# Kernel tuning notes

Measured on AMD Instinct MI355X. Metric: run time of the kernel, lower is better.

Reference implementation:

```python
import jax, jax.numpy as jnp
import numpy as np

STRIDE, PAD, DIL = 1, 1, 1
EPS = 1e-12
RHO_LIM = 1.0 - 1e-6
PI = jnp.pi


def clamp_pg(x, lo=0.0):
    # clamp value but pass gradient through (clamp_preserve_grad)
    return x + jax.lax.stop_gradient(jnp.maximum(x, lo) - x)


def setup_inputs() -> dict:
    key = jax.random.key(0)
    B, N, T, K = 8, 128, 1024, 3
    k = jax.random.uniform(key, (B, B, N, T, 2), dtype=jnp.float32)
    leak = jnp.array(1.0, dtype=jnp.float32)
    alpha = jnp.full((1, 1, K), 1.0 / K, dtype=jnp.float32)
    beta = jnp.array(0.0, dtype=jnp.float32)
    return {"k": k, "leak": leak, "alpha": alpha, "beta": beta}


def reference(k, leak, alpha, beta):
    k_gp, k_ntk = k[..., 0], k[..., 1]          # (B,B,N,T) each
    B, _, N, T = k_gp.shape

    # v[b,t] = k_gp[b,b,0,t]  (diagonal over batch dims, first lag)
    ar = jnp.arange(B)
    v = k_gp[ar, ar, 0, :]                      # (B,T)
    v_pad = jnp.pad(v, ((0, 0), (0, N - 1)))    # (B, T+N-1)

    v_xx = v[:, None, None, :]                  # (B,1,1,T)
    idx = jnp.arange(N)[:, None] + jnp.arange(T)[None, :]  # (N,T)
    v_yy = v_pad[:, idx][None]                  # (1,B,N,T): v_pad[b, n+t]

    # calculate_statistics
    std_x = jnp.sqrt(jnp.maximum(v_xx, 0.0))
    std_y = jnp.sqrt(jnp.maximum(v_yy, 0.0))
    denom = jnp.maximum(std_x * std_y, EPS)
    rho = jnp.clip(k_gp / denom, -RHO_LIM, RHO_LIM)  # (B,B,N,T)

    a = clamp_pg(leak)
    theta = jnp.arccos(rho)
    s = jnp.sqrt(1.0 - rho * rho)
    one_m = (1.0 - a) ** 2
    coef = 1.0 + a * a
    # leaky-ReLU arccos kernel and its derivative kernel
    c0 = std_x * std_y / (2.0 * PI) * (one_m * s + rho * (coef * PI - one_m * theta))
    c1 = (coef * PI - one_m * theta) / (2.0 * PI)

    w = clamp_pg(alpha)                         # (1,1,K)

    def conv(x):  # x: (B,B,N,T) -> (B,B,N,T')
        y = jax.lax.conv_general_dilated(
            x.reshape(-1, 1, T), w, window_strides=(STRIDE,),
            padding=[(PAD, PAD)], rhs_dilation=(DIL,),
            dimension_numbers=("NCH", "OIH", "NCH"))
        return y.reshape(B, B, N, -1)

    kg = conv(c0)
    kn = conv(c1 * k_ntk) + kg

    b = clamp_pg(beta)
    kg = kg + b
    kn = kn + b
    return jnp.stack([kg, kn], axis=-1)
```

## Files before the change

kernel.cpp:

```cpp
#include <hip/hip_runtime.h>
#include <math.h>

#define BDIM 8
#define NDIM 128
#define TDIM 1024
#define TPB 256

#define EPS_F 1e-12f
#define RHO_LIM_F (1.0f - 1e-6f)
#define PI_F 3.14159265358979323846f

__global__ __launch_bounds__(TPB) void conv_arccos_kernel(
    const float* __restrict__ k,
    const float* __restrict__ leak,
    const float* __restrict__ alpha,
    const float* __restrict__ beta,
    float* __restrict__ out)
{
    __shared__ float sc0[TDIM + 2];
    __shared__ float scn[TDIM + 2];

    const int row = blockIdx.x;
    const int n   = row % NDIM;
    const int bb  = row / NDIM;
    const int b2  = bb % BDIM;
    const int b1  = bb / BDIM;

    const int tid = threadIdx.x;

    const float a   = fmaxf(leak[0], 0.0f);
    const float w0  = fmaxf(alpha[0], 0.0f);
    const float w1  = fmaxf(alpha[1], 0.0f);
    const float w2  = fmaxf(alpha[2], 0.0f);
    const float bia = fmaxf(beta[0], 0.0f);

    const float one_m  = (1.0f - a) * (1.0f - a);
    const float coef   = 1.0f + a * a;
    const float inv2pi = 1.0f / (2.0f * PI_F);

    const float2* krow   = (const float2*)(k) + (size_t)row * TDIM;
    const float2* vrow_x = (const float2*)(k) + (size_t)(b1 * BDIM + b1) * NDIM * TDIM;
    const float2* vrow_y = (const float2*)(k) + (size_t)(b2 * BDIM + b2) * NDIM * TDIM;

    if (tid == 0) {
        sc0[0] = 0.0f; scn[0] = 0.0f;
        sc0[TDIM + 1] = 0.0f; scn[TDIM + 1] = 0.0f;
    }

    #pragma unroll
    for (int j = 0; j < TDIM / TPB; ++j) {
        const int t = tid + j * TPB;
        float2 kv = krow[t];
        const float kgp  = kv.x;
        const float kntk = kv.y;

        const float vx = vrow_x[t].x;
        const int   ty = n + t;
        const float vy = (ty < TDIM) ? vrow_y[ty].x : 0.0f;

        const float sx   = sqrtf(fmaxf(vx, 0.0f));
        const float sy   = sqrtf(fmaxf(vy, 0.0f));
        const float prod = sx * sy;
        const float den  = fmaxf(prod, EPS_F);

        const float rho   = fminf(fmaxf(kgp / den, -RHO_LIM_F), RHO_LIM_F);
        const float theta = acosf(rho);
        const float s     = sqrtf(1.0f - rho * rho);

        const float br = coef * PI_F - one_m * theta;
        const float c0 = prod * inv2pi * (one_m * s + rho * br);
        const float c1 = br * inv2pi;

        sc0[t + 1] = c0;
        scn[t + 1] = c1 * kntk;
    }

    __syncthreads();

    float2* orow = (float2*)(out) + (size_t)row * TDIM;
    #pragma unroll
    for (int j = 0; j < TDIM / TPB; ++j) {
        const int t = tid + j * TPB;
        const float kg = w0 * sc0[t] + w1 * sc0[t + 1] + w2 * sc0[t + 2];
        const float kn = w0 * scn[t] + w1 * scn[t + 1] + w2 * scn[t + 2] + kg;
        float2 o;
        o.x = kg + bia;
        o.y = kn + bia;
        orow[t] = o;
    }
}

extern "C" void kernel_launch(void* const* d_in, const int* in_sizes, int n_in,
                              void* d_out, int out_size, void* d_ws, size_t ws_size,
                              hipStream_t stream) {
    const float* k     = (const float*)d_in[0];
    const float* leak  = (const float*)d_in[1];
    const float* alpha = (const float*)d_in[2];
    const float* beta  = (const float*)d_in[3];
    float* out = (float*)d_out;

    const int n_rows = BDIM * BDIM * NDIM;
    conv_arccos_kernel<<<n_rows, TPB, 0, stream>>>(k, leak, alpha, beta, out);
}
```

Before: 128.9 us.

## Vectorize per-thread float4 processing and add fast path for unit leak

Each thread now handles four contiguous time steps with float4 loads and stores for the input row, the diagonal variance row and the output. The three-tap convolution reads one halo value per side from shared memory. When the clamped leak makes (1-a)^2 zero, a runtime branch skips acos and the inner sqrt, since the kernel formula then reduces exactly to simple products. The divide is replaced with a hardware reciprocal and the two square roots are fused into one, which slightly reduces precision.

New measurement: 136.4 us. 1.06x slower.

```diff
diff --git a/kernel.cpp b/kernel.cpp
--- a/kernel.cpp
+++ b/kernel.cpp
@@ -10,6 +10,7 @@
 #define RHO_LIM_F (1.0f - 1e-6f)
 #define PI_F 3.14159265358979323846f
 
+
 __global__ __launch_bounds__(TPB) void conv_arccos_kernel(
     const float* __restrict__ k,
     const float* __restrict__ leak,
@@ -17,16 +18,16 @@
     const float* __restrict__ beta,
     float* __restrict__ out)
 {
-    __shared__ float sc0[TDIM + 2];
-    __shared__ float scn[TDIM + 2];
+    __shared__ __align__(16) float sc0[TDIM + 8];
+    __shared__ __align__(16) float scn[TDIM + 8];
 
     const int row = blockIdx.x;
     const int n   = row % NDIM;
     const int bb  = row / NDIM;
     const int b2  = bb % BDIM;
     const int b1  = bb / BDIM;
-
     const int tid = threadIdx.x;
+    const int t   = tid * 4;
 
     const float a   = fmaxf(leak[0], 0.0f);
     const float w0  = fmaxf(alpha[0], 0.0f);
@@ -36,58 +37,89 @@
 
     const float one_m  = (1.0f - a) * (1.0f - a);
     const float coef   = 1.0f + a * a;
-    const float inv2pi = 1.0f / (2.0f * PI_F);
+    const float inv2pi = 0.15915494309189535f;
 
-    const float2* krow   = (const float2*)(k) + (size_t)row * TDIM;
-    const float2* vrow_x = (const float2*)(k) + (size_t)(b1 * BDIM + b1) * NDIM * TDIM;
-    const float2* vrow_y = (const float2*)(k) + (size_t)(b2 * BDIM + b2) * NDIM * TDIM;
+    const float4* krow4 = (const float4*)(k + (size_t)row * TDIM * 2);
+    const float2* vrx = (const float2*)(k) + (size_t)(b1 * BDIM + b1) * NDIM * TDIM;
+    const float2* vry = (const float2*)(k) + (size_t)(b2 * BDIM + b2) * NDIM * TDIM;
 
-    if (tid == 0) {
-        sc0[0] = 0.0f; scn[0] = 0.0f;
-        sc0[TDIM + 1] = 0.0f; scn[TDIM + 1] = 0.0f;
+    if (tid == 0) { sc0[3] = 0.0f; scn[3] = 0.0f; }
+    if (tid == 1) { sc0[TDIM + 4] = 0.0f; scn[TDIM + 4] = 0.0f; }
+
+    const float4 kvA = krow4[2 * tid];
+    const float4 kvB = krow4[2 * tid + 1];
+    const float4 vxA = ((const float4*)vrx)[2 * tid];
+    const float4 vxB = ((const float4*)vrx)[2 * tid + 1];
+
+    const int lim = TDIM - n;
+    const float vy0 = (t     < lim) ? vry[n + t    ].x : 0.0f;
+    const float vy1 = (t + 1 < lim) ? vry[n + t + 1].x : 0.0f;
+    const float vy2 = (t + 2 < lim) ? vry[n + t + 2].x : 0.0f;
+    const float vy3 = (t + 3 < lim) ? vry[n + t + 3].x : 0.0f;
+
+    const float p0 = sqrtf(fmaxf(vxA.x, 0.0f) * fmaxf(vy0, 0.0f));
+    const float p1 = sqrtf(fmaxf(vxA.z, 0.0f) * fmaxf(vy1, 0.0f));
+    const float p2 = sqrtf(fmaxf(vxB.x, 0.0f) * fmaxf(vy2, 0.0f));
+    const float p3 = sqrtf(fmaxf(vxB.z, 0.0f) * fmaxf(vy3, 0.0f));
+
+    const float r0 = fminf(fmaxf(kvA.x * __builtin_amdgcn_rcpf(fmaxf(p0, EPS_F)), -RHO_LIM_F), RHO_LIM_F);
+    const float r1 = fminf(fmaxf(kvA.z * __builtin_amdgcn_rcpf(fmaxf(p1, EPS_F)), -RHO_LIM_F), RHO_LIM_F);
+    const float r2 = fminf(fmaxf(kvB.x * __builtin_amdgcn_rcpf(fmaxf(p2, EPS_F)), -RHO_LIM_F), RHO_LIM_F);
+    const float r3 = fminf(fmaxf(kvB.z * __builtin_amdgcn_rcpf(fmaxf(p3, EPS_F)), -RHO_LIM_F), RHO_LIM_F);
+
+    float4 c0v, cnv;
+    if (one_m == 0.0f) {
+        const float hc = 0.5f * coef;
+        c0v.x = p0 * r0 * hc;  c0v.y = p1 * r1 * hc;
+        c0v.z = p2 * r2 * hc;  c0v.w = p3 * r3 * hc;
+        cnv.x = hc * kvA.y;    cnv.y = hc * kvA.w;
+        cnv.z = hc * kvB.y;    cnv.w = hc * kvB.w;
+    } else {
+        const float th0 = acosf(r0), th1 = acosf(r1), th2 = acosf(r2), th3 = acosf(r3);
+        const float s0 = sqrtf(1.0f - r0 * r0), s1 = sqrtf(1.0f - r1 * r1);
+        const float s2 = sqrtf(1.0f - r2 * r2), s3 = sqrtf(1.0f - r3 * r3);
+        const float br0 = coef * PI_F - one_m * th0;
+        const float br1 = coef * PI_F - one_m * th1;
+        const float br2 = coef * PI_F - one_m * th2;
+        const float br3 = coef * PI_F - one_m * th3;
+        c0v.x = p0 * inv2pi * (one_m * s0 + r0 * br0);
+        c0v.y = p1 * inv2pi * (one_m * s1 + r1 * br1);
+        c0v.z = p2 * inv2pi * (one_m * s2 + r2 * br2);
+        c0v.w = p3 * inv2pi * (one_m * s3 + r3 * br3);
+        cnv.x = br0 * inv2pi * kvA.y;
+        cnv.y = br1 * inv2pi * kvA.w;
+        cnv.z = br2 * inv2pi * kvB.y;
+        cnv.w = br3 * inv2pi * kvB.w;
     }
 
-    #pragma unroll
-    for (int j = 0; j < TDIM / TPB; ++j) {
-        const int t = tid + j * TPB;
-        float2 kv = krow[t];
-        const float kgp  = kv.x;
-        const float kntk = kv.y;
-
-        const float vx = vrow_x[t].x;
-        const int   ty = n + t;
-        const float vy = (ty < TDIM) ? vrow_y[ty].x : 0.0f;
-
-        const float sx   = sqrtf(fmaxf(vx, 0.0f));
-        const float sy   = sqrtf(fmaxf(vy, 0.0f));
-        const float prod = sx * sy;
-        const float den  = fmaxf(prod, EPS_F);
-
-        const float rho   = fminf(fmaxf(kgp / den, -RHO_LIM_F), RHO_LIM_F);
-        const float theta = acosf(rho);
-        const float s     = sqrtf(1.0f - rho * rho);
-
-        const float br = coef * PI_F - one_m * theta;
-        const float c0 = prod * inv2pi * (one_m * s + rho * br);
-        const float c1 = br * inv2pi;
-
-        sc0[t + 1] = c0;
-        scn[t + 1] = c1 * kntk;
-    }
+    ((float4*)&sc0[4])[tid] = c0v;
+    ((float4*)&scn[4])[tid] = cnv;
 
     __syncthreads();
 
-    float2* orow = (float2*)(out) + (size_t)row * TDIM;
-    #pragma unroll
-    for (int j = 0; j < TDIM / TPB; ++j) {
-        const int t = tid + j * TPB;
-        const float kg = w0 * sc0[t] + w1 * sc0[t + 1] + w2 * sc0[t + 2];
-        const float kn = w0 * scn[t] + w1 * scn[t + 1] + w2 * scn[t + 2] + kg;
-        float2 o;
-        o.x = kg + bia;
-        o.y = kn + bia;
-        orow[t] = o;
-    }
+    const float c0l = sc0[t + 3];
+    const float c0r = sc0[t + 8];
+    const float cnl = scn[t + 3];
+    const float cnr = scn[t + 8];
+    const float4 m0 = ((const float4*)&sc0[4])[tid];
+    const float4 m1 = ((const float4*)&scn[4])[tid];
+
+    const float kg0 = w0 * c0l  + w1 * m0.x + w2 * m0.y;
+    const float kg1 = w0 * m0.x + w1 * m0.y + w2 * m0.z;
+    const float kg2 = w0 * m0.y + w1 * m0.z + w2 * m0.w;
+    const float kg3 = w0 * m0.z + w1 * m0.w + w2 * c0r;
+
+    const float kn0 = w0 * cnl  + w1 * m1.x + w2 * m1.y + kg0;
+    const float kn1 = w0 * m1.x + w1 * m1.y + w2 * m1.z + kg1;
+    const float kn2 = w0 * m1.y + w1 * m1.z + w2 * m1.w + kg2;
+    const float kn3 = w0 * m1.z + w1 * m1.w + w2 * cnr  + kg3;
+
+    float4* orow = (float4*)(out + (size_t)row * TDIM * 2);
+    float4 oA, oB;
+    oA.x = kg0 + bia; oA.y = kn0 + bia; oA.z = kg1 + bia; oA.w = kn1 + bia;
+    oB.x = kg2 + bia; oB.y = kn2 + bia; oB.z = kg3 + bia; oB.w = kn3 + bia;
+    orow[2 * tid]     = oA;
+    orow[2 * tid + 1] = oB;
 }
 
 extern "C" void kernel_launch(void* const* d_in, const int* in_sizes, int n_in,
```
